# Optimization experiments

Hardware: AMD Instinct MI355X
Metric: run time of the kernel (lower is better)

## Reference

```python
import jax, jax.numpy as jnp
import numpy as np
import math

IN_DIM = 512
OUT_DIM = 512
GRID_SIZE = 8
SPLINE_ORDER = 3
N_COEFFS = GRID_SIZE + SPLINE_ORDER          # 11
N_KNOTS = GRID_SIZE + 2 * SPLINE_ORDER + 1   # 15
BATCH = 16384


def setup_inputs() -> dict:
    key = jax.random.key(0)
    k_x, k_c, k_w = jax.random.split(key, 3)
    x = jax.random.uniform(k_x, (BATCH, IN_DIM), dtype=jnp.float32, minval=-1.0, maxval=1.0)
    coeffs = 0.1 * jax.random.normal(k_c, (OUT_DIM, IN_DIM, N_COEFFS), dtype=jnp.float32)
    # kaiming_uniform_(a=sqrt(5)) on [out,in]: bound = sqrt(6 / ((1 + 5) * in)) = 1/sqrt(in)
    bound = 1.0 / math.sqrt(IN_DIM)
    base_weight = jax.random.uniform(k_w, (OUT_DIM, IN_DIM), dtype=jnp.float32, minval=-bound, maxval=bound)
    step = 2.0 / GRID_SIZE
    grid_steps_log = jnp.full((IN_DIM, N_KNOTS - 1), math.log(step), dtype=jnp.float32)
    grid_start = jnp.full((IN_DIM, 1), -1.0 - step * SPLINE_ORDER, dtype=jnp.float32)
    res_scale = jnp.zeros((1,), dtype=jnp.float32)
    return {"x": x, "coeffs": coeffs, "base_weight": base_weight,
            "grid_steps_log": grid_steps_log, "grid_start": grid_start,
            "res_scale": res_scale}


def _get_grid(grid_steps_log, grid_start):
    steps = jax.nn.softplus(grid_steps_log)                   # (in, n_knots-1)
    offsets = jnp.cumsum(steps, axis=1)
    return jnp.concatenate([grid_start, grid_start + offsets], axis=1)  # (in, n_knots)


def _b_spline(x, grid):
    # x: (b, in) -> bases: (b, in, n_coeffs) via Cox-de Boor recursion
    xe = x[..., None]                                         # (b, in, 1)
    bases = ((xe >= grid[:, :-1]) & (xe < grid[:, 1:])).astype(x.dtype)
    for k in range(1, SPLINE_ORDER + 1):
        left_den = grid[:, k:-1] - grid[:, :-(k + 1)]
        left = (xe - grid[:, :-(k + 1)]) / jnp.where(left_den == 0, 1.0, left_den)
        right_den = grid[:, k + 1:] - grid[:, 1:-k]
        right = (grid[:, k + 1:] - xe) / jnp.where(right_den == 0, 1.0, right_den)
        bases = left * bases[..., :-1] + right * bases[..., 1:]
    return bases


def reference(x, coeffs, base_weight, grid_steps_log, grid_start, res_scale):
    grid = _get_grid(grid_steps_log, grid_start)
    spline_basis = _b_spline(x, grid)                         # (b, in, n_coeffs)
    spline_out = jnp.einsum('oic,bic->bo', coeffs, spline_basis)
    base_out = jax.nn.silu(x) @ base_weight.T                 # (b, out)
    y = spline_out + base_out + res_scale * x                 # residual (in_dim==out_dim)
    return jnp.tanh(y)
```

## Files before the change

### kernel.cpp

```cpp
#include <hip/hip_runtime.h>
#include <hip/hip_bf16.h>
#include <math.h>


#define IN_DIM  512
#define OUT_DIM 512
#define FPI     12
#define KTOT    (IN_DIM * FPI)
#define NBATCH  16384

#define P_SLOTS     56
#define WS_WH_OFF_F (P_SLOTS * IN_DIM)
#define WS_F_OFF_B  ((size_t)(P_SLOTS * IN_DIM * 4) + (size_t)OUT_DIM * KTOT * 2)

typedef _Float16 half8 __attribute__((ext_vector_type(8)));
typedef float f32x4 __attribute__((ext_vector_type(4)));

__device__ __forceinline__ void gload16(const void* g, void* l) {
    __builtin_amdgcn_global_load_lds((const __attribute__((address_space(1))) void*)g,
                                     (__attribute__((address_space(3))) void*)l, 16, 0, 0);
}

__global__ void kan_prep(const float* __restrict__ gsl, const float* __restrict__ gstart,
                         float* __restrict__ P) {
    int i = blockIdx.x * 256 + threadIdx.x;
    if (i >= IN_DIM) return;
    float t[15];
    float a = gstart[i];
    t[0] = a;
#pragma unroll
    for (int m = 0; m < 14; ++m) {
        float z = gsl[i * 14 + m];
        a += fmaxf(z, 0.f) + log1pf(__expf(-fabsf(z)));
        t[m + 1] = a;
    }
#pragma unroll
    for (int m = 0; m < 15; ++m) P[m * IN_DIM + i] = t[m];
#pragma unroll
    for (int m = 0; m < 14; ++m) { float d = t[m+1] - t[m]; P[(15+m)*IN_DIM + i] = 1.f / ((d == 0.f) ? 1.f : d); }
#pragma unroll
    for (int m = 0; m < 13; ++m) { float d = t[m+2] - t[m]; P[(29+m)*IN_DIM + i] = 1.f / ((d == 0.f) ? 1.f : d); }
#pragma unroll
    for (int m = 0; m < 12; ++m) { float d = t[m+3] - t[m]; P[(42+m)*IN_DIM + i] = 1.f / ((d == 0.f) ? 1.f : d); }
}

__global__ void kan_packw(const float* __restrict__ coeffs, const float* __restrict__ bw,
                          _Float16* __restrict__ Wh) {
    int idx = blockIdx.x * 256 + threadIdx.x;
    const float* src = coeffs + (size_t)idx * 11;
    union { _Float16 h[12]; float2 f2[3]; } u;
#pragma unroll
    for (int c = 0; c < 11; ++c) u.h[c] = (_Float16)src[c];
    u.h[11] = (_Float16)bw[idx];
    float2* dst = (float2*)(Wh + (size_t)idx * FPI);
    dst[0] = u.f2[0]; dst[1] = u.f2[1]; dst[2] = u.f2[2];
}

__launch_bounds__(256)
__global__ void kan_feat(const float* __restrict__ x, const float* __restrict__ P,
                         _Float16* __restrict__ F, int row0) {
    const int dim = (blockIdx.x & 1) * 256 + threadIdx.x;
    const int rb = blockIdx.x >> 1;
    float t[15], i1[14], i2[13], i3[12];
#pragma unroll
    for (int m = 0; m < 15; ++m) t[m]  = P[m * IN_DIM + dim];
#pragma unroll
    for (int m = 0; m < 14; ++m) i1[m] = P[(15 + m) * IN_DIM + dim];
#pragma unroll
    for (int m = 0; m < 13; ++m) i2[m] = P[(29 + m) * IN_DIM + dim];
#pragma unroll
    for (int m = 0; m < 12; ++m) i3[m] = P[(42 + m) * IN_DIM + dim];
    const int lr0 = rb * 32;
#pragma unroll 2
    for (int rr = 0; rr < 32; ++rr) {
        const int lr = lr0 + rr;
        const float xv = x[(size_t)(row0 + lr) * IN_DIM + dim];
        float d[15];
#pragma unroll
        for (int m = 0; m < 15; ++m) d[m] = xv - t[m];
        float b[14];
#pragma unroll
        for (int m = 0; m < 14; ++m) b[m] = (xv >= t[m] && xv < t[m + 1]) ? 1.f : 0.f;
#pragma unroll
        for (int m = 0; m < 13; ++m) b[m] = (d[m] * i1[m]) * b[m] + ((-d[m + 2]) * i1[m + 1]) * b[m + 1];
#pragma unroll
        for (int m = 0; m < 12; ++m) b[m] = (d[m] * i2[m]) * b[m] + ((-d[m + 3]) * i2[m + 1]) * b[m + 1];
#pragma unroll
        for (int m = 0; m < 11; ++m) b[m] = (d[m] * i3[m]) * b[m] + ((-d[m + 4]) * i3[m + 1]) * b[m + 1];
        const float sil = xv / (1.f + __expf(-xv));
        union { _Float16 h[12]; float2 f2[3]; } u;
#pragma unroll
        for (int c = 0; c < 11; ++c) u.h[c] = (_Float16)b[c];
        u.h[11] = (_Float16)sil;
        float2* dst = (float2*)(F + (size_t)lr * KTOT + dim * FPI);
        dst[0] = u.f2[0]; dst[1] = u.f2[1]; dst[2] = u.f2[2];
    }
}

__launch_bounds__(256, 2)
__global__ void kan_gemm(const _Float16* __restrict__ F, const _Float16* __restrict__ Wh,
                         const float* __restrict__ x, const float* __restrict__ rsp,
                         float* __restrict__ out, int row0) {
    __shared__ _Float16 As[128 * 32];
    __shared__ _Float16 Bs[128 * 32];
    int bid = blockIdx.x;
    const int nwg = gridDim.x;
    if ((nwg & 7) == 0) bid = (bid & 7) * (nwg >> 3) + (bid >> 3);
    const int rt = bid >> 2, ct = bid & 3;
    const int lr0 = rt * 128, o0 = ct * 128;
    const int tid = threadIdx.x, l = tid & 63, w = tid >> 6;
    const int wr = (w >> 1) * 64, wc = (w & 1) * 64;

    f32x4 acc[4][4];
    const f32x4 zz = {0.f, 0.f, 0.f, 0.f};
#pragma unroll
    for (int m = 0; m < 4; ++m)
#pragma unroll
        for (int n = 0; n < 4; ++n) acc[m][n] = zz;

    const int srow = tid >> 2;
    const int sbo = (tid & 3) * 8;
    const _Float16* gA = F  + (size_t)(lr0 + srow) * KTOT + sbo;
    const _Float16* gB = Wh + (size_t)(o0 + srow) * KTOT + sbo;
    _Float16* lA = As + tid * 8;
    _Float16* lB = Bs + tid * 8;

    const int ar = wr + (l & 15), br = wc + (l & 15), ko = (l >> 4) * 8;

    for (int s = 0; s < KTOT / 32; ++s) {
        const int k0 = s * 32;
        gload16(gA + k0, lA);
        gload16(gA + k0 + (size_t)64 * KTOT, lA + 64 * 32);
        gload16(gB + k0, lB);
        gload16(gB + k0 + (size_t)64 * KTOT, lB + 64 * 32);
        __syncthreads();
        half8 af[4], bf[4];
#pragma unroll
        for (int m = 0; m < 4; ++m) af[m] = *(const half8*)&As[(ar + m * 16) * 32 + ko];
#pragma unroll
        for (int n = 0; n < 4; ++n) bf[n] = *(const half8*)&Bs[(br + n * 16) * 32 + ko];
#pragma unroll
        for (int m = 0; m < 4; ++m)
#pragma unroll
            for (int n = 0; n < 4; ++n)
                acc[m][n] = __builtin_amdgcn_mfma_f32_16x16x32_f16(af[m], bf[n], acc[m][n], 0, 0, 0);
        __syncthreads();
    }

    const float rs = rsp[0];
#pragma unroll
    for (int m = 0; m < 4; ++m)
#pragma unroll
        for (int n = 0; n < 4; ++n)
#pragma unroll
            for (int j = 0; j < 4; ++j) {
                const int r = row0 + lr0 + wr + m * 16 + (l >> 4) * 4 + j;
                const int c = o0 + wc + n * 16 + (l & 15);
                float v = acc[m][n][j] + rs * x[(size_t)r * IN_DIM + c];
                float e = __expf(2.f * v);
                out[(size_t)r * OUT_DIM + c] = 1.f - 2.f / (e + 1.f);
            }
}

extern "C" void kernel_launch(void* const* d_in, const int* in_sizes, int n_in,
                              void* d_out, int out_size, void* d_ws, size_t ws_size,
                              hipStream_t stream) {
    const float* x      = (const float*)d_in[0];
    const float* coeffs = (const float*)d_in[1];
    const float* bw     = (const float*)d_in[2];
    const float* gsl    = (const float*)d_in[3];
    const float* gstart = (const float*)d_in[4];
    const float* rs     = (const float*)d_in[5];
    float* out = (float*)d_out;
    float* P   = (float*)d_ws;
    _Float16* Wh = (_Float16*)(P + WS_WH_OFF_F);
    _Float16* F  = (_Float16*)((char*)d_ws + WS_F_OFF_B);

    kan_prep<<<2, 256, 0, stream>>>(gsl, gstart, P);
    kan_packw<<<1024, 256, 0, stream>>>(coeffs, bw, Wh);

    int CH = NBATCH;
    while (CH > 128 && WS_F_OFF_B + (size_t)CH * KTOT * 2 > ws_size) CH >>= 1;
    if (WS_F_OFF_B + (size_t)CH * KTOT * 2 > ws_size) return;

    for (int row0 = 0; row0 < NBATCH; row0 += CH) {
        kan_feat<<<2 * (CH / 32), 256, 0, stream>>>(x, P, F, row0);
        kan_gemm<<<(CH / 128) * 4, 256, 0, stream>>>(F, Wh, x, rs, out, row0);
    }
}
```

Before: 323.4 us.

## Double-buffer GEMM LDS tiles and stage feature writes through shared memory

The GEMM main loop now uses two LDS buffers, so global-to-LDS loads for the next K step are issued before the MFMAs on the current step, hiding load latency. The feature kernel now handles 8 rows per block and stages its fp16 output in LDS, then writes it with coalesced 16-byte stores in place of strided 8-byte stores. This doubles GEMM LDS use, which may cut occupancy, and gives the feature kernel more blocks that each reload the grid parameters.

```diff
diff --git a/kernel.cpp b/kernel.cpp
--- a/kernel.cpp
+++ b/kernel.cpp
@@ -56,11 +56,15 @@
     dst[0] = u.f2[0]; dst[1] = u.f2[1]; dst[2] = u.f2[2];
 }
 
+#define FR 8
 __launch_bounds__(256)
 __global__ void kan_feat(const float* __restrict__ x, const float* __restrict__ P,
                          _Float16* __restrict__ F, int row0) {
-    const int dim = (blockIdx.x & 1) * 256 + threadIdx.x;
+    __shared__ __align__(16) _Float16 Ft[FR][3072];
+    const int tid = threadIdx.x;
+    const int half = blockIdx.x & 1;
     const int rb = blockIdx.x >> 1;
+    const int dim = half * 256 + tid;
     float t[15], i1[14], i2[13], i3[12];
 #pragma unroll
     for (int m = 0; m < 15; ++m) t[m]  = P[m * IN_DIM + dim];
@@ -70,11 +74,10 @@
     for (int m = 0; m < 13; ++m) i2[m] = P[(29 + m) * IN_DIM + dim];
 #pragma unroll
     for (int m = 0; m < 12; ++m) i3[m] = P[(42 + m) * IN_DIM + dim];
-    const int lr0 = rb * 32;
+    const int r0 = row0 + rb * FR;
 #pragma unroll 2
-    for (int rr = 0; rr < 32; ++rr) {
-        const int lr = lr0 + rr;
-        const float xv = x[(size_t)(row0 + lr) * IN_DIM + dim];
+    for (int r = 0; r < FR; ++r) {
+        const float xv = x[(size_t)(r0 + r) * IN_DIM + dim];
         float d[15];
 #pragma unroll
         for (int m = 0; m < 15; ++m) d[m] = xv - t[m];
@@ -92,17 +95,27 @@
 #pragma unroll
         for (int c = 0; c < 11; ++c) u.h[c] = (_Float16)b[c];
         u.h[11] = (_Float16)sil;
-        float2* dst = (float2*)(F + (size_t)lr * KTOT + dim * FPI);
+        float2* dst = (float2*)&Ft[r][tid * FPI];
         dst[0] = u.f2[0]; dst[1] = u.f2[1]; dst[2] = u.f2[2];
     }
-}
-
+    __syncthreads();
+#pragma unroll
+    for (int rd = 0; rd < 12; ++rd) {
+        const int ci = rd * 256 + tid;
+        const int row = ci / 384;
+        const int off = (ci - row * 384) * 8;
+        float4 v = *(const float4*)&Ft[row][off];
+        *(float4*)(F + (size_t)(r0 + row) * KTOT + half * 3072 + off) = v;
+    }
+}
+
+#define NS (KTOT / 32)
 __launch_bounds__(256, 2)
 __global__ void kan_gemm(const _Float16* __restrict__ F, const _Float16* __restrict__ Wh,
                          const float* __restrict__ x, const float* __restrict__ rsp,
                          float* __restrict__ out, int row0) {
-    __shared__ _Float16 As[128 * 32];
-    __shared__ _Float16 Bs[128 * 32];
+    __shared__ _Float16 As[2][128 * 32];
+    __shared__ _Float16 Bs[2][128 * 32];
     int bid = blockIdx.x;
     const int nwg = gridDim.x;
     if ((nwg & 7) == 0) bid = (bid & 7) * (nwg >> 3) + (bid >> 3);
@@ -122,29 +135,39 @@
     const int sbo = (tid & 3) * 8;
     const _Float16* gA = F  + (size_t)(lr0 + srow) * KTOT + sbo;
     const _Float16* gB = Wh + (size_t)(o0 + srow) * KTOT + sbo;
-    _Float16* lA = As + tid * 8;
-    _Float16* lB = Bs + tid * 8;
 
     const int ar = wr + (l & 15), br = wc + (l & 15), ko = (l >> 4) * 8;
 
-    for (int s = 0; s < KTOT / 32; ++s) {
-        const int k0 = s * 32;
-        gload16(gA + k0, lA);
-        gload16(gA + k0 + (size_t)64 * KTOT, lA + 64 * 32);
-        gload16(gB + k0, lB);
-        gload16(gB + k0 + (size_t)64 * KTOT, lB + 64 * 32);
-        __syncthreads();
+    {
+        gload16(gA, &As[0][tid * 8]);
+        gload16(gA + (size_t)64 * KTOT, &As[0][64 * 32 + tid * 8]);
+        gload16(gB, &Bs[0][tid * 8]);
+        gload16(gB + (size_t)64 * KTOT, &Bs[0][64 * 32 + tid * 8]);
+    }
+    __syncthreads();
+
+    int cur = 0;
+    for (int s = 0; s < NS; ++s) {
+        if (s + 1 < NS) {
+            const int k1 = (s + 1) * 32;
+            const int nb = cur ^ 1;
+            gload16(gA + k1, &As[nb][tid * 8]);
+            gload16(gA + k1 + (size_t)64 * KTOT, &As[nb][64 * 32 + tid * 8]);
+            gload16(gB + k1, &Bs[nb][tid * 8]);
+            gload16(gB + k1 + (size_t)64 * KTOT, &Bs[nb][64 * 32 + tid * 8]);
+        }
         half8 af[4], bf[4];
 #pragma unroll
-        for (int m = 0; m < 4; ++m) af[m] = *(const half8*)&As[(ar + m * 16) * 32 + ko];
-#pragma unroll
-        for (int n = 0; n < 4; ++n) bf[n] = *(const half8*)&Bs[(br + n * 16) * 32 + ko];
+        for (int m = 0; m < 4; ++m) af[m] = *(const half8*)&As[cur][(ar + m * 16) * 32 + ko];
+#pragma unroll
+        for (int n = 0; n < 4; ++n) bf[n] = *(const half8*)&Bs[cur][(br + n * 16) * 32 + ko];
 #pragma unroll
         for (int m = 0; m < 4; ++m)
 #pragma unroll
             for (int n = 0; n < 4; ++n)
                 acc[m][n] = __builtin_amdgcn_mfma_f32_16x16x32_f16(af[m], bf[n], acc[m][n], 0, 0, 0);
         __syncthreads();
+        cur ^= 1;
     }
 
     const float rs = rsp[0];
@@ -184,7 +207,7 @@
     if (WS_F_OFF_B + (size_t)CH * KTOT * 2 > ws_size) return;
 
     for (int row0 = 0; row0 < NBATCH; row0 += CH) {
-        kan_feat<<<2 * (CH / 32), 256, 0, stream>>>(x, P, F, row0);
+        kan_feat<<<2 * (CH / FR), 256, 0, stream>>>(x, P, F, row0);
         kan_gemm<<<(CH / 128) * 4, 256, 0, stream>>>(F, Wh, x, rs, out, row0);
     }
 }
```

Measured after the change: 322.5 us. About the same (-0.3%).

## Fuse B-spline feature generation into the fp16 MFMA GEMM kernel

Applied to the files above, without the earlier changes.

Removes the separate feature kernel and its large fp16 feature matrix round-trip through global memory. Each 128x256 GEMM block now computes the B-spline bases and SiLU for 8 input dims per K step directly into LDS, while the packed weights stream in via global_load_lds. The knot parameters are relaid out per dim with a 64-float stride, and the block now uses 512 threads. The cost is that each K step must finish basis computation before the MFMAs, with no double buffering. The spline features are also recomputed by both column tiles.

```diff
diff --git a/kernel.cpp b/kernel.cpp
--- a/kernel.cpp
+++ b/kernel.cpp
@@ -9,12 +9,19 @@
 #define KTOT    (IN_DIM * FPI)
 #define NBATCH  16384
 
-#define P_SLOTS     56
-#define WS_WH_OFF_F (P_SLOTS * IN_DIM)
-#define WS_F_OFF_B  ((size_t)(P_SLOTS * IN_DIM * 4) + (size_t)OUT_DIM * KTOT * 2)
+#define PSTRIDE 64
+#define WS_WH_OFF_F (PSTRIDE * IN_DIM)
+
+#define BMF 128
+#define BNF 256
+#define KS  96
+#define LDA 104
+#define NSTEPS 64
 
 typedef _Float16 half8 __attribute__((ext_vector_type(8)));
+typedef _Float16 half4 __attribute__((ext_vector_type(4)));
 typedef float f32x4 __attribute__((ext_vector_type(4)));
+typedef float f32x2 __attribute__((ext_vector_type(2)));
 
 __device__ __forceinline__ void gload16(const void* g, void* l) {
     __builtin_amdgcn_global_load_lds((const __attribute__((address_space(1))) void*)g,
@@ -34,14 +41,17 @@
         a += fmaxf(z, 0.f) + log1pf(__expf(-fabsf(z)));
         t[m + 1] = a;
     }
-#pragma unroll
-    for (int m = 0; m < 15; ++m) P[m * IN_DIM + i] = t[m];
-#pragma unroll
-    for (int m = 0; m < 14; ++m) { float d = t[m+1] - t[m]; P[(15+m)*IN_DIM + i] = 1.f / ((d == 0.f) ? 1.f : d); }
-#pragma unroll
-    for (int m = 0; m < 13; ++m) { float d = t[m+2] - t[m]; P[(29+m)*IN_DIM + i] = 1.f / ((d == 0.f) ? 1.f : d); }
-#pragma unroll
-    for (int m = 0; m < 12; ++m) { float d = t[m+3] - t[m]; P[(42+m)*IN_DIM + i] = 1.f / ((d == 0.f) ? 1.f : d); }
+    float* p = P + (size_t)i * PSTRIDE;
+#pragma unroll
+    for (int m = 0; m < 15; ++m) p[m] = t[m];
+#pragma unroll
+    for (int m = 0; m < 14; ++m) { float d = t[m+1] - t[m]; p[15+m] = 1.f / ((d == 0.f) ? 1.f : d); }
+#pragma unroll
+    for (int m = 0; m < 13; ++m) { float d = t[m+2] - t[m]; p[29+m] = 1.f / ((d == 0.f) ? 1.f : d); }
+#pragma unroll
+    for (int m = 0; m < 12; ++m) { float d = t[m+3] - t[m]; p[42+m] = 1.f / ((d == 0.f) ? 1.f : d); }
+#pragma unroll
+    for (int m = 54; m < 64; ++m) p[m] = 0.f;
 }
 
 __global__ void kan_packw(const float* __restrict__ coeffs, const float* __restrict__ bw,
@@ -56,60 +66,23 @@
     dst[0] = u.f2[0]; dst[1] = u.f2[1]; dst[2] = u.f2[2];
 }
 
-__launch_bounds__(256)
-__global__ void kan_feat(const float* __restrict__ x, const float* __restrict__ P,
-                         _Float16* __restrict__ F, int row0) {
-    const int dim = (blockIdx.x & 1) * 256 + threadIdx.x;
-    const int rb = blockIdx.x >> 1;
-    float t[15], i1[14], i2[13], i3[12];
-#pragma unroll
-    for (int m = 0; m < 15; ++m) t[m]  = P[m * IN_DIM + dim];
-#pragma unroll
-    for (int m = 0; m < 14; ++m) i1[m] = P[(15 + m) * IN_DIM + dim];
-#pragma unroll
-    for (int m = 0; m < 13; ++m) i2[m] = P[(29 + m) * IN_DIM + dim];
-#pragma unroll
-    for (int m = 0; m < 12; ++m) i3[m] = P[(42 + m) * IN_DIM + dim];
-    const int lr0 = rb * 32;
-#pragma unroll 2
-    for (int rr = 0; rr < 32; ++rr) {
-        const int lr = lr0 + rr;
-        const float xv = x[(size_t)(row0 + lr) * IN_DIM + dim];
-        float d[15];
-#pragma unroll
-        for (int m = 0; m < 15; ++m) d[m] = xv - t[m];
-        float b[14];
-#pragma unroll
-        for (int m = 0; m < 14; ++m) b[m] = (xv >= t[m] && xv < t[m + 1]) ? 1.f : 0.f;
-#pragma unroll
-        for (int m = 0; m < 13; ++m) b[m] = (d[m] * i1[m]) * b[m] + ((-d[m + 2]) * i1[m + 1]) * b[m + 1];
-#pragma unroll
-        for (int m = 0; m < 12; ++m) b[m] = (d[m] * i2[m]) * b[m] + ((-d[m + 3]) * i2[m + 1]) * b[m + 1];
-#pragma unroll
-        for (int m = 0; m < 11; ++m) b[m] = (d[m] * i3[m]) * b[m] + ((-d[m + 4]) * i3[m + 1]) * b[m + 1];
-        const float sil = xv / (1.f + __expf(-xv));
-        union { _Float16 h[12]; float2 f2[3]; } u;
-#pragma unroll
-        for (int c = 0; c < 11; ++c) u.h[c] = (_Float16)b[c];
-        u.h[11] = (_Float16)sil;
-        float2* dst = (float2*)(F + (size_t)lr * KTOT + dim * FPI);
-        dst[0] = u.f2[0]; dst[1] = u.f2[1]; dst[2] = u.f2[2];
-    }
-}
-
-__launch_bounds__(256, 2)
-__global__ void kan_gemm(const _Float16* __restrict__ F, const _Float16* __restrict__ Wh,
-                         const float* __restrict__ x, const float* __restrict__ rsp,
-                         float* __restrict__ out, int row0) {
-    __shared__ _Float16 As[128 * 32];
-    __shared__ _Float16 Bs[128 * 32];
-    int bid = blockIdx.x;
-    const int nwg = gridDim.x;
-    if ((nwg & 7) == 0) bid = (bid & 7) * (nwg >> 3) + (bid >> 3);
-    const int rt = bid >> 2, ct = bid & 3;
-    const int lr0 = rt * 128, o0 = ct * 128;
-    const int tid = threadIdx.x, l = tid & 63, w = tid >> 6;
-    const int wr = (w >> 1) * 64, wc = (w & 1) * 64;
+__launch_bounds__(512, 4)
+__global__ void kan_fused(const float* __restrict__ x, const float* __restrict__ P,
+                          const _Float16* __restrict__ Wh, const float* __restrict__ rsp,
+                          float* __restrict__ out) {
+    __shared__ __align__(16) _Float16 Al[BMF][LDA];
+    __shared__ __align__(16) _Float16 Bl[BNF][KS];
+    __shared__ __align__(16) float    xl[BMF][10];
+
+    const int tid = threadIdx.x;
+    const int l = tid & 63;
+    const int w = __builtin_amdgcn_readfirstlane(tid >> 6);
+    const int bid = blockIdx.x;
+    const int rt = bid >> 1, ct = bid & 1;
+    const int b0 = rt * BMF, o0 = ct * BNF;
+
+    const int wr = (w >> 2) * 64;
+    const int wc = (w & 3) * 64;
 
     f32x4 acc[4][4];
     const f32x4 zz = {0.f, 0.f, 0.f, 0.f};
@@ -118,32 +91,100 @@
 #pragma unroll
         for (int n = 0; n < 4; ++n) acc[m][n] = zz;
 
-    const int srow = tid >> 2;
-    const int sbo = (tid & 3) * 8;
-    const _Float16* gA = F  + (size_t)(lr0 + srow) * KTOT + sbo;
-    const _Float16* gB = Wh + (size_t)(o0 + srow) * KTOT + sbo;
-    _Float16* lA = As + tid * 8;
-    _Float16* lB = Bs + tid * 8;
-
-    const int ar = wr + (l & 15), br = wc + (l & 15), ko = (l >> 4) * 8;
-
-    for (int s = 0; s < KTOT / 32; ++s) {
-        const int k0 = s * 32;
-        gload16(gA + k0, lA);
-        gload16(gA + k0 + (size_t)64 * KTOT, lA + 64 * 32);
-        gload16(gB + k0, lB);
-        gload16(gB + k0 + (size_t)64 * KTOT, lB + 64 * 32);
+    int ofsB[6];
+#pragma unroll
+    for (int i = 0; i < 6; ++i) {
+        int c = tid + i * 512;
+        int row = c / 12, off = c - row * 12;
+        ofsB[i] = ((o0 + row) * KTOT + off * 8) * 2;
+    }
+    char* BlFlat = (char*)&Bl[0][0];
+
+    if (tid < 256) {
+        int row = tid >> 1, part = tid & 1;
+        float4 v = *(const float4*)&x[(size_t)(b0 + row) * IN_DIM + part * 4];
+        *(f32x2*)&xl[row][part * 4]     = f32x2{v.x, v.y};
+        *(f32x2*)&xl[row][part * 4 + 2] = f32x2{v.z, v.w};
+    }
+    __syncthreads();
+
+    for (int s = 0; s < NSTEPS; ++s) {
+#pragma unroll
+        for (int i = 0; i < 6; ++i)
+            gload16((const char*)Wh + (ofsB[i] + s * (KS * 2)), BlFlat + tid * 16 + i * 8192);
+
+        {
+            const float* ps = P + (size_t)(s * 8 + w) * PSTRIDE;
+            f32x2 X = { xl[l][w], xl[l + 64][w] };
+            f32x2 b[14];
+#pragma unroll
+            for (int m = 0; m < 14; ++m) {
+                float tm = ps[m], tm1 = ps[m + 1];
+                b[m].x = (X.x >= tm && X.x < tm1) ? 1.f : 0.f;
+                b[m].y = (X.y >= tm && X.y < tm1) ? 1.f : 0.f;
+            }
+#pragma unroll
+            for (int m = 0; m < 13; ++m) {
+                f32x2 dm = X - ps[m];
+                f32x2 dp = X - ps[m + 2];
+                b[m] = (dm * ps[15 + m]) * b[m] - (dp * ps[16 + m]) * b[m + 1];
+            }
+#pragma unroll
+            for (int m = 0; m < 12; ++m) {
+                f32x2 dm = X - ps[m];
+                f32x2 dp = X - ps[m + 3];
+                b[m] = (dm * ps[29 + m]) * b[m] - (dp * ps[30 + m]) * b[m + 1];
+            }
+#pragma unroll
+            for (int m = 0; m < 11; ++m) {
+                f32x2 dm = X - ps[m];
+                f32x2 dp = X - ps[m + 4];
+                b[m] = (dm * ps[42 + m]) * b[m] - (dp * ps[43 + m]) * b[m + 1];
+            }
+            f32x2 sil;
+            sil.x = X.x / (1.f + __expf(-X.x));
+            sil.y = X.y / (1.f + __expf(-X.y));
+#pragma unroll
+            for (int pt = 0; pt < 2; ++pt) {
+                const int row = l + pt * 64;
+#define BC(m) (pt ? b[m].y : b[m].x)
+                half4 h0 = { (_Float16)BC(0), (_Float16)BC(1), (_Float16)BC(2), (_Float16)BC(3) };
+                half4 h1 = { (_Float16)BC(4), (_Float16)BC(5), (_Float16)BC(6), (_Float16)BC(7) };
+                half4 h2 = { (_Float16)BC(8), (_Float16)BC(9), (_Float16)BC(10),
+                             (_Float16)(pt ? sil.y : sil.x) };
+#undef BC
+                *(half4*)&Al[row][w * 12]     = h0;
+                *(half4*)&Al[row][w * 12 + 4] = h1;
+                *(half4*)&Al[row][w * 12 + 8] = h2;
+            }
+        }
         __syncthreads();
-        half8 af[4], bf[4];
-#pragma unroll
-        for (int m = 0; m < 4; ++m) af[m] = *(const half8*)&As[(ar + m * 16) * 32 + ko];
-#pragma unroll
-        for (int n = 0; n < 4; ++n) bf[n] = *(const half8*)&Bs[(br + n * 16) * 32 + ko];
-#pragma unroll
-        for (int m = 0; m < 4; ++m)
-#pragma unroll
-            for (int n = 0; n < 4; ++n)
-                acc[m][n] = __builtin_amdgcn_mfma_f32_16x16x32_f16(af[m], bf[n], acc[m][n], 0, 0, 0);
+
+        if (s + 1 < NSTEPS && tid < 256) {
+            int row = tid >> 1, part = tid & 1;
+            float4 v = *(const float4*)&x[(size_t)(b0 + row) * IN_DIM + (s + 1) * 8 + part * 4];
+            *(f32x2*)&xl[row][part * 4]     = f32x2{v.x, v.y};
+            *(f32x2*)&xl[row][part * 4 + 2] = f32x2{v.z, v.w};
+        }
+
+        {
+            const int ar = wr + (l & 15);
+            const int bc = wc + (l & 15);
+            const int ko = (l >> 4) * 8;
+#pragma unroll
+            for (int kk = 0; kk < 3; ++kk) {
+                half8 af[4], bf[4];
+#pragma unroll
+                for (int m = 0; m < 4; ++m) af[m] = *(const half8*)&Al[ar + m * 16][kk * 32 + ko];
+#pragma unroll
+                for (int n = 0; n < 4; ++n) bf[n] = *(const half8*)&Bl[bc + n * 16][kk * 32 + ko];
+#pragma unroll
+                for (int m = 0; m < 4; ++m)
+#pragma unroll
+                    for (int n = 0; n < 4; ++n)
+                        acc[m][n] = __builtin_amdgcn_mfma_f32_16x16x32_f16(af[m], bf[n], acc[m][n], 0, 0, 0);
+            }
+        }
         __syncthreads();
     }
 
@@ -154,7 +195,7 @@
         for (int n = 0; n < 4; ++n)
 #pragma unroll
             for (int j = 0; j < 4; ++j) {
-                const int r = row0 + lr0 + wr + m * 16 + (l >> 4) * 4 + j;
+                const int r = b0 + wr + m * 16 + (l >> 4) * 4 + j;
                 const int c = o0 + wc + n * 16 + (l & 15);
                 float v = acc[m][n][j] + rs * x[(size_t)r * IN_DIM + c];
                 float e = __expf(2.f * v);
@@ -174,17 +215,8 @@
     float* out = (float*)d_out;
     float* P   = (float*)d_ws;
     _Float16* Wh = (_Float16*)(P + WS_WH_OFF_F);
-    _Float16* F  = (_Float16*)((char*)d_ws + WS_F_OFF_B);
 
     kan_prep<<<2, 256, 0, stream>>>(gsl, gstart, P);
     kan_packw<<<1024, 256, 0, stream>>>(coeffs, bw, Wh);
-
-    int CH = NBATCH;
-    while (CH > 128 && WS_F_OFF_B + (size_t)CH * KTOT * 2 > ws_size) CH >>= 1;
-    if (WS_F_OFF_B + (size_t)CH * KTOT * 2 > ws_size) return;
-
-    for (int row0 = 0; row0 < NBATCH; row0 += CH) {
-        kan_feat<<<2 * (CH / 32), 256, 0, stream>>>(x, P, F, row0);
-        kan_gemm<<<(CH / 128) * 4, 256, 0, stream>>>(F, Wh, x, rs, out, row0);
-    }
-}
+    kan_fused<<<(NBATCH / BMF) * (OUT_DIM / BNF), 512, 0, stream>>>(x, P, Wh, rs, out);
+}
```

After: 401.1 us. +24.0%, slower.

## Stage KAN feature writes through LDS and widen GEMM K-tile with swizzled LDS

Applied to the files above, without the earlier changes.

The feature kernel now handles 64 rows by 16 dims per step in 1024-thread blocks. It stages x and the fp16 features in shared memory so global writes become coalesced 16-byte stores, and the per-dim spline parameters are laid out contiguously (stride 64) so each wave reads one dim's params uniformly. The GEMM K tile doubles from 32 to 64 with an XOR-swizzled LDS layout, which halves the number of barriers per K and is meant to avoid bank conflicts on the half8 fragment reads. In exchange the feature kernel adds barriers and does per-lane redundant reads of the parameters, and the GEMM uses more LDS per block.

```diff
diff --git a/kernel.cpp b/kernel.cpp
--- a/kernel.cpp
+++ b/kernel.cpp
@@ -9,11 +9,12 @@
 #define KTOT    (IN_DIM * FPI)
 #define NBATCH  16384
 
-#define P_SLOTS     56
-#define WS_WH_OFF_F (P_SLOTS * IN_DIM)
-#define WS_F_OFF_B  ((size_t)(P_SLOTS * IN_DIM * 4) + (size_t)OUT_DIM * KTOT * 2)
+#define PSTRIDE 64
+#define WS_WH_OFF_F (PSTRIDE * IN_DIM)
+#define WS_F_OFF_B  ((size_t)(PSTRIDE * IN_DIM * 4) + (size_t)OUT_DIM * KTOT * 2)
 
 typedef _Float16 half8 __attribute__((ext_vector_type(8)));
+typedef _Float16 half4 __attribute__((ext_vector_type(4)));
 typedef float f32x4 __attribute__((ext_vector_type(4)));
 
 __device__ __forceinline__ void gload16(const void* g, void* l) {
@@ -34,14 +35,17 @@
         a += fmaxf(z, 0.f) + log1pf(__expf(-fabsf(z)));
         t[m + 1] = a;
     }
-#pragma unroll
-    for (int m = 0; m < 15; ++m) P[m * IN_DIM + i] = t[m];
-#pragma unroll
-    for (int m = 0; m < 14; ++m) { float d = t[m+1] - t[m]; P[(15+m)*IN_DIM + i] = 1.f / ((d == 0.f) ? 1.f : d); }
-#pragma unroll
-    for (int m = 0; m < 13; ++m) { float d = t[m+2] - t[m]; P[(29+m)*IN_DIM + i] = 1.f / ((d == 0.f) ? 1.f : d); }
-#pragma unroll
-    for (int m = 0; m < 12; ++m) { float d = t[m+3] - t[m]; P[(42+m)*IN_DIM + i] = 1.f / ((d == 0.f) ? 1.f : d); }
+    float* p = P + (size_t)i * PSTRIDE;
+#pragma unroll
+    for (int m = 0; m < 15; ++m) p[m] = t[m];
+#pragma unroll
+    for (int m = 0; m < 14; ++m) { float d = t[m+1] - t[m]; p[15+m] = 1.f / ((d == 0.f) ? 1.f : d); }
+#pragma unroll
+    for (int m = 0; m < 13; ++m) { float d = t[m+2] - t[m]; p[29+m] = 1.f / ((d == 0.f) ? 1.f : d); }
+#pragma unroll
+    for (int m = 0; m < 12; ++m) { float d = t[m+3] - t[m]; p[42+m] = 1.f / ((d == 0.f) ? 1.f : d); }
+#pragma unroll
+    for (int m = 54; m < 64; ++m) p[m] = 0.f;
 }
 
 __global__ void kan_packw(const float* __restrict__ coeffs, const float* __restrict__ bw,
@@ -56,53 +60,68 @@
     dst[0] = u.f2[0]; dst[1] = u.f2[1]; dst[2] = u.f2[2];
 }
 
-__launch_bounds__(256)
+__launch_bounds__(1024, 4)
 __global__ void kan_feat(const float* __restrict__ x, const float* __restrict__ P,
                          _Float16* __restrict__ F, int row0) {
-    const int dim = (blockIdx.x & 1) * 256 + threadIdx.x;
-    const int rb = blockIdx.x >> 1;
-    float t[15], i1[14], i2[13], i3[12];
-#pragma unroll
-    for (int m = 0; m < 15; ++m) t[m]  = P[m * IN_DIM + dim];
-#pragma unroll
-    for (int m = 0; m < 14; ++m) i1[m] = P[(15 + m) * IN_DIM + dim];
-#pragma unroll
-    for (int m = 0; m < 13; ++m) i2[m] = P[(29 + m) * IN_DIM + dim];
-#pragma unroll
-    for (int m = 0; m < 12; ++m) i3[m] = P[(42 + m) * IN_DIM + dim];
-    const int lr0 = rb * 32;
-#pragma unroll 2
-    for (int rr = 0; rr < 32; ++rr) {
-        const int lr = lr0 + rr;
-        const float xv = x[(size_t)(row0 + lr) * IN_DIM + dim];
-        float d[15];
-#pragma unroll
-        for (int m = 0; m < 15; ++m) d[m] = xv - t[m];
-        float b[14];
-#pragma unroll
-        for (int m = 0; m < 14; ++m) b[m] = (xv >= t[m] && xv < t[m + 1]) ? 1.f : 0.f;
-#pragma unroll
-        for (int m = 0; m < 13; ++m) b[m] = (d[m] * i1[m]) * b[m] + ((-d[m + 2]) * i1[m + 1]) * b[m + 1];
-#pragma unroll
-        for (int m = 0; m < 12; ++m) b[m] = (d[m] * i2[m]) * b[m] + ((-d[m + 3]) * i2[m + 1]) * b[m + 1];
-#pragma unroll
-        for (int m = 0; m < 11; ++m) b[m] = (d[m] * i3[m]) * b[m] + ((-d[m + 4]) * i3[m + 1]) * b[m + 1];
-        const float sil = xv / (1.f + __expf(-xv));
-        union { _Float16 h[12]; float2 f2[3]; } u;
-#pragma unroll
-        for (int c = 0; c < 11; ++c) u.h[c] = (_Float16)b[c];
-        u.h[11] = (_Float16)sil;
-        float2* dst = (float2*)(F + (size_t)lr * KTOT + dim * FPI);
-        dst[0] = u.f2[0]; dst[1] = u.f2[1]; dst[2] = u.f2[2];
-    }
-}
-
+    __shared__ float xl[64][17];
+    __shared__ __align__(16) _Float16 Fl[64][208];
+    const int tid = threadIdx.x;
+    const int l = tid & 63;
+    const int w = __builtin_amdgcn_readfirstlane(tid >> 6);
+    const int r0 = row0 + blockIdx.x * 64;
+
+    for (int ss = 0; ss < 32; ++ss) {
+        const int d0 = ss * 16;
+        {
+            const int row = tid >> 4, col = tid & 15;
+            xl[row][col] = x[(size_t)(r0 + row) * IN_DIM + d0 + col];
+        }
+        __syncthreads();
+        {
+            const float* ps = P + (size_t)(d0 + w) * PSTRIDE;
+            const float X = xl[l][w];
+            float b[14];
+#pragma unroll
+            for (int m = 0; m < 14; ++m)
+                b[m] = (X >= ps[m] && X < ps[m + 1]) ? 1.f : 0.f;
+#pragma unroll
+            for (int m = 0; m < 13; ++m)
+                b[m] = ((X - ps[m]) * ps[15 + m]) * b[m] + ((ps[m + 2] - X) * ps[16 + m]) * b[m + 1];
+#pragma unroll
+            for (int m = 0; m < 12; ++m)
+                b[m] = ((X - ps[m]) * ps[29 + m]) * b[m] + ((ps[m + 3] - X) * ps[30 + m]) * b[m + 1];
+#pragma unroll
+            for (int m = 0; m < 11; ++m)
+                b[m] = ((X - ps[m]) * ps[42 + m]) * b[m] + ((ps[m + 4] - X) * ps[43 + m]) * b[m + 1];
+            const float sil = X / (1.f + __expf(-X));
+            half4 h0 = { (_Float16)b[0], (_Float16)b[1], (_Float16)b[2],  (_Float16)b[3] };
+            half4 h1 = { (_Float16)b[4], (_Float16)b[5], (_Float16)b[6],  (_Float16)b[7] };
+            half4 h2 = { (_Float16)b[8], (_Float16)b[9], (_Float16)b[10], (_Float16)sil  };
+            *(half4*)&Fl[l][w * 12]     = h0;
+            *(half4*)&Fl[l][w * 12 + 4] = h1;
+            *(half4*)&Fl[l][w * 12 + 8] = h2;
+        }
+        __syncthreads();
+#pragma unroll
+        for (int rr = 0; rr < 2; ++rr) {
+            int ci = tid + rr * 1024;
+            if (ci < 1536) {
+                int row = ci / 24, c16 = ci - row * 24;
+                float4 v = *(const float4*)&Fl[row][c16 * 8];
+                *(float4*)((char*)F + (size_t)(r0 + row) * (KTOT * 2) + (size_t)d0 * 24 + c16 * 16) = v;
+            }
+        }
+    }
+}
+
+#define BKH 64
+#define NS2 (KTOT / BKH)
 __launch_bounds__(256, 2)
 __global__ void kan_gemm(const _Float16* __restrict__ F, const _Float16* __restrict__ Wh,
                          const float* __restrict__ x, const float* __restrict__ rsp,
                          float* __restrict__ out, int row0) {
-    __shared__ _Float16 As[128 * 32];
-    __shared__ _Float16 Bs[128 * 32];
+    __shared__ __align__(16) _Float16 As[128 * BKH];
+    __shared__ __align__(16) _Float16 Bs[128 * BKH];
     int bid = blockIdx.x;
     const int nwg = gridDim.x;
     if ((nwg & 7) == 0) bid = (bid & 7) * (nwg >> 3) + (bid >> 3);
@@ -118,32 +137,44 @@
 #pragma unroll
         for (int n = 0; n < 4; ++n) acc[m][n] = zz;
 
-    const int srow = tid >> 2;
-    const int sbo = (tid & 3) * 8;
-    const _Float16* gA = F  + (size_t)(lr0 + srow) * KTOT + sbo;
-    const _Float16* gB = Wh + (size_t)(o0 + srow) * KTOT + sbo;
-    _Float16* lA = As + tid * 8;
-    _Float16* lB = Bs + tid * 8;
-
-    const int ar = wr + (l & 15), br = wc + (l & 15), ko = (l >> 4) * 8;
-
-    for (int s = 0; s < KTOT / 32; ++s) {
-        const int k0 = s * 32;
-        gload16(gA + k0, lA);
-        gload16(gA + k0 + (size_t)64 * KTOT, lA + 64 * 32);
-        gload16(gB + k0, lB);
-        gload16(gB + k0 + (size_t)64 * KTOT, lB + 64 * 32);
-        __syncthreads();
-        half8 af[4], bf[4];
-#pragma unroll
-        for (int m = 0; m < 4; ++m) af[m] = *(const half8*)&As[(ar + m * 16) * 32 + ko];
-#pragma unroll
-        for (int n = 0; n < 4; ++n) bf[n] = *(const half8*)&Bs[(br + n * 16) * 32 + ko];
-#pragma unroll
-        for (int m = 0; m < 4; ++m)
+    const char* pA[4];
+    const char* pB[4];
+#pragma unroll
+    for (int r = 0; r < 4; ++r) {
+        const int lam = r * 256 + tid;
+        const int row = lam >> 3;
+        const int scol = ((lam ^ (lam >> 3)) & 7) * 16;
+        pA[r] = (const char*)F  + (size_t)(row0 + lr0 + row) * (KTOT * 2) + scol;
+        pB[r] = (const char*)Wh + (size_t)(o0 + row) * (KTOT * 2) + scol;
+    }
+
+    const int xv = (l & 7) << 4;
+    const int arow = wr + (l & 15), brow = wc + (l & 15);
+
+    for (int s = 0; s < NS2; ++s) {
+        const int kb = s * 128;
+#pragma unroll
+        for (int r = 0; r < 4; ++r) {
+            gload16(pA[r] + kb, (char*)As + (r * 256 + tid) * 16);
+            gload16(pB[r] + kb, (char*)Bs + (r * 256 + tid) * 16);
+        }
+        __syncthreads();
+#pragma unroll
+        for (int kk = 0; kk < 2; ++kk) {
+            const int colb = ((kk * 64) | ((l >> 4) * 16)) ^ xv;
+            half8 af[4], bf[4];
+#pragma unroll
+            for (int m = 0; m < 4; ++m)
+                af[m] = *(const half8*)((const char*)As + (arow + m * 16) * 128 + colb);
 #pragma unroll
             for (int n = 0; n < 4; ++n)
-                acc[m][n] = __builtin_amdgcn_mfma_f32_16x16x32_f16(af[m], bf[n], acc[m][n], 0, 0, 0);
+                bf[n] = *(const half8*)((const char*)Bs + (brow + n * 16) * 128 + colb);
+#pragma unroll
+            for (int m = 0; m < 4; ++m)
+#pragma unroll
+                for (int n = 0; n < 4; ++n)
+                    acc[m][n] = __builtin_amdgcn_mfma_f32_16x16x32_f16(af[m], bf[n], acc[m][n], 0, 0, 0);
+        }
         __syncthreads();
     }
 
@@ -184,7 +215,7 @@
     if (WS_F_OFF_B + (size_t)CH * KTOT * 2 > ws_size) return;
 
     for (int row0 = 0; row0 < NBATCH; row0 += CH) {
-        kan_feat<<<2 * (CH / 32), 256, 0, stream>>>(x, P, F, row0);
+        kan_feat<<<CH / 64, 1024, 0, stream>>>(x, P, F, row0);
         kan_gemm<<<(CH / 128) * 4, 256, 0, stream>>>(F, Wh, x, rs, out, row0);
     }
 }
```

After: 303.9 us. -6.0%, faster.
